# Kernel tuning notes

Measured on AMD Instinct MI355X. Metric: run time of the kernel, lower is better.

The kernel has to match this reference:

```python
import jax, jax.numpy as jnp
import numpy as np

N_NODES = 100000
N_EDGES = 1600000
IN_DIM = 128
HID = 128
OUT = 40


def setup_inputs() -> dict:
    key = jax.random.key(0)
    ks = jax.random.split(key, 8)
    x = jax.random.normal(ks[0], (N_NODES, IN_DIM), dtype=jnp.float32)
    edge_index = jax.random.randint(ks[1], (2, N_EDGES), 0, N_NODES, dtype=jnp.int64)
    def glorot(k, fan_in, fan_out):
        s = jnp.sqrt(6.0 / (fan_in + fan_out)).astype(jnp.float32)
        return jax.random.uniform(k, (fan_in, fan_out), jnp.float32, -s, s)
    return {
        "x": x,
        "edge_index": edge_index,
        "W1": glorot(ks[2], IN_DIM, HID), "b1": jnp.zeros((HID,), jnp.float32),
        "W2": glorot(ks[3], HID, HID),    "b2": jnp.zeros((HID,), jnp.float32),
        "W3": glorot(ks[4], HID, HID),    "b3": jnp.zeros((HID,), jnp.float32),
        "Wl": glorot(ks[5], HID, OUT),    "bl": jnp.zeros((OUT,), jnp.float32),
    }


def _gcn_norm(edge_index, num_nodes):
    # PyG GCNConv default: add self-loops, symmetric normalization.
    loops = jnp.arange(num_nodes, dtype=edge_index.dtype)
    src = jnp.concatenate([edge_index[0], loops])
    dst = jnp.concatenate([edge_index[1], loops])
    deg = jax.ops.segment_sum(jnp.ones_like(dst, dtype=jnp.float32), dst,
                              num_segments=num_nodes)
    dis = jnp.where(deg > 0, jax.lax.rsqrt(deg), 0.0)  # deg^{-1/2}
    norm = dis[src] * dis[dst]  # [E+N]
    return src, dst, norm


def _gcn_conv(x, W, b, src, dst, norm, num_nodes):
    h = x @ W                                   # [N, F_out]
    msg = h[src] * norm[:, None]                # gather + scale
    out = jax.ops.segment_sum(msg, dst, num_segments=num_nodes)
    return out + b


def reference(x, edge_index, W1, b1, W2, b2, W3, b3, Wl, bl):
    n = x.shape[0]
    src, dst, norm = _gcn_norm(edge_index, n)
    h = jax.nn.relu(_gcn_conv(x, W1, b1, src, dst, norm, n))
    h = jax.nn.relu(_gcn_conv(h, W2, b2, src, dst, norm, n))
    h = _gcn_conv(h, W3, b3, src, dst, norm, n)
    # dropout p=0.5 is identity in eval mode
    return h @ Wl + bl
```

## Files before the change

kernel.cpp:

```cpp
#include <hip/hip_runtime.h>

typedef __attribute__((ext_vector_type(8))) short sh8;
typedef __attribute__((ext_vector_type(4))) float f4;

__device__ __forceinline__ float bf2f(unsigned short u) {
    union { unsigned int u; float f; } c; c.u = ((unsigned int)u) << 16; return c.f;
}
__device__ __forceinline__ unsigned short f2bf(float f) {
    union { float f; unsigned int u; } c; c.f = f;
    unsigned int x = c.u;
    unsigned int r = (x + 0x7fffu + ((x >> 16) & 1u)) >> 16;
    return (unsigned short)r;
}
__device__ __forceinline__ void bfsplit(float x, short& hi, short& lo) {
    unsigned short h = f2bf(x);
    float r = x - bf2f(h);
    hi = (short)h;
    lo = (short)f2bf(r);
}

#define CG_BLOCKS 2304
#define CG_COUNT  1152
#define CSR_GRID  1568

__global__ void k_init(int* cnt8, int M,
                       const float* __restrict__ W1, const float* __restrict__ W2,
                       const float* __restrict__ W3, unsigned short* __restrict__ sp) {
    int j = blockIdx.x * 256 + threadIdx.x;
    if (j < M) cnt8[j] = 0;
    if (j < 16384) {
        int k = j >> 7, col = j & 127;
        int t = col * 128 + k;
        short h, l;
        bfsplit(W1[j], h, l); sp[t] = (unsigned short)h; sp[16384 + t] = (unsigned short)l;
        bfsplit(W2[j], h, l); sp[32768 + t] = (unsigned short)h; sp[49152 + t] = (unsigned short)l;
        bfsplit(W3[j], h, l); sp[65536 + t] = (unsigned short)h; sp[81920 + t] = (unsigned short)l;
    }
}

__device__ __forceinline__ void count_body(const int* __restrict__ dst,
                                           int* __restrict__ cnt8,
                                           int* __restrict__ rank, int E, int N) {
    int cidx = blockIdx.x >> 1;
    int base = (cidx & 7) * N;
    int E4 = E >> 2;
    for (int i = cidx * 256 + threadIdx.x; i < E4; i += CG_COUNT * 256) {
        int4 d = ((const int4*)dst)[i];
        int4 r;
        r.x = ((unsigned)d.x < (unsigned)N) ? atomicAdd(&cnt8[base + d.x], 1) : -1;
        r.y = ((unsigned)d.y < (unsigned)N) ? atomicAdd(&cnt8[base + d.y], 1) : -1;
        r.z = ((unsigned)d.z < (unsigned)N) ? atomicAdd(&cnt8[base + d.z], 1) : -1;
        r.w = ((unsigned)d.w < (unsigned)N) ? atomicAdd(&cnt8[base + d.w], 1) : -1;
        ((int4*)rank)[i] = r;
    }
    if (cidx == 0) {
        for (int e = (E4 << 2) + threadIdx.x; e < E; e += 256) {
            int d = dst[e];
            rank[e] = ((unsigned)d < (unsigned)N) ? atomicAdd(&cnt8[d], 1) : -1;
        }
    }
}

__device__ __forceinline__ void gemm1_body(const float* __restrict__ X,
                                           const unsigned short* __restrict__ Wh,
                                           const unsigned short* __restrict__ Wl,
                                           unsigned short* __restrict__ H, int nPairs) {
    int gidx = blockIdx.x >> 1;
    int wave = threadIdx.x >> 6;
    int lane = threadIdx.x & 63;
    int ln = lane & 15, quad = lane >> 4;
    int c0 = (wave & 1) * 64;
    int subTile = wave >> 1;

    for (int p = gidx; p < nPairs; p += CG_COUNT) {
        int nodeBase = p * 32 + subTile * 16;
        const float* xrow = X + (nodeBase + ln) * 128 + quad * 8;
        sh8 ah[4], al[4];
        #pragma unroll
        for (int kt = 0; kt < 4; ++kt) {
            f4 v0 = *(const f4*)(xrow + kt * 32);
            f4 v1 = *(const f4*)(xrow + kt * 32 + 4);
            #pragma unroll
            for (int j = 0; j < 4; ++j) {
                short h, l;
                bfsplit(v0[j], h, l); ah[kt][j] = h; al[kt][j] = l;
                bfsplit(v1[j], h, l); ah[kt][j + 4] = h; al[kt][j + 4] = l;
            }
        }

        f4 acc[4] = { {0.f,0.f,0.f,0.f}, {0.f,0.f,0.f,0.f}, {0.f,0.f,0.f,0.f}, {0.f,0.f,0.f,0.f} };
        #pragma unroll
        for (int kt = 0; kt < 4; ++kt) {
            int k0 = kt * 32 + quad * 8;
            #pragma unroll
            for (int nt = 0; nt < 4; ++nt) {
                int col = c0 + nt * 16 + ln;
                sh8 bh = *(const sh8*)(Wh + col * 128 + k0);
                sh8 bl = *(const sh8*)(Wl + col * 128 + k0);
                acc[nt] = __builtin_amdgcn_mfma_f32_16x16x32_bf16(ah[kt], bh, acc[nt], 0, 0, 0);
                acc[nt] = __builtin_amdgcn_mfma_f32_16x16x32_bf16(ah[kt], bl, acc[nt], 0, 0, 0);
                acc[nt] = __builtin_amdgcn_mfma_f32_16x16x32_bf16(al[kt], bh, acc[nt], 0, 0, 0);
            }
        }

        #pragma unroll
        for (int nt = 0; nt < 4; ++nt) {
            int col = c0 + nt * 16 + ln;
            #pragma unroll
            for (int r = 0; r < 4; ++r)
                H[(nodeBase + quad * 4 + r) * 128 + col] = f2bf(acc[nt][r]);
        }
    }
}

__global__ __launch_bounds__(256)
void k_count_gemm1(const int* __restrict__ dst, int* __restrict__ cnt8,
                   int* __restrict__ rank, int E, int N,
                   const float* __restrict__ X,
                   const unsigned short* __restrict__ Wh,
                   const unsigned short* __restrict__ Wl,
                   unsigned short* __restrict__ H, int nPairs) {
    if ((blockIdx.x & 1) == 0)
        count_body(dst, cnt8, rank, E, N);
    else
        gemm1_body(X, Wh, Wl, H, nPairs);
}

#define SCAN_B 256
__global__ void k_scan_a(const int* __restrict__ cnt8, int* __restrict__ rowptr,
                         int* __restrict__ off8, int* __restrict__ deg,
                         int* __restrict__ bsum, float* __restrict__ dis, int N) {
    __shared__ int sh[SCAN_B];
    int t = threadIdx.x, i = blockIdx.x * SCAN_B + t;
    int c[8];
    int v = 0;
    if (i < N) {
        #pragma unroll
        for (int g = 0; g < 8; ++g) { c[g] = cnt8[g * N + i]; v += c[g]; }
        dis[i] = rsqrtf((float)(v + 1));
        deg[i] = v;
    }
    sh[t] = v; __syncthreads();
    for (int off = 1; off < SCAN_B; off <<= 1) {
        int x = (t >= off) ? sh[t - off] : 0;
        __syncthreads();
        sh[t] += x;
        __syncthreads();
    }
    int incl = sh[t];
    if (i < N) {
        int b = incl - v;
        rowptr[i] = b;
        int o = b;
        #pragma unroll
        for (int g = 0; g < 8; ++g) { off8[g * N + i] = o; o += c[g]; }
    }
    if (t == SCAN_B - 1) bsum[blockIdx.x] = incl;
}

__global__ void k_scan_b(int* bsum, int NB) {
    __shared__ int sh[512];
    int t = threadIdx.x;
    int v = (t < NB) ? bsum[t] : 0;
    sh[t] = v; __syncthreads();
    for (int off = 1; off < 512; off <<= 1) {
        int x = (t >= off) ? sh[t - off] : 0;
        __syncthreads();
        sh[t] += x;
        __syncthreads();
    }
    if (t < NB) bsum[t] = sh[t] - v;
}

__global__ void k_scan_c(int* __restrict__ rowptr, int* __restrict__ off8,
                         const int* __restrict__ bsum, int N) {
    int i = blockIdx.x * 256 + threadIdx.x;
    if (i < N) {
        int b = bsum[blockIdx.x];
        rowptr[i] += b;
        #pragma unroll
        for (int g = 0; g < 8; ++g) off8[g * N + i] += b;
    }
}

__global__ void k_fill(const int* __restrict__ src, const int* __restrict__ dst,
                       const int* __restrict__ rank, const int* __restrict__ off8,
                       int* __restrict__ csrc, int E, int N) {
    int E4 = E >> 2;
    for (int i = blockIdx.x * 256 + threadIdx.x; i < E4; i += gridDim.x * 256) {
        int g = (i >> 8) & 7;
        const int* off = off8 + g * N;
        int4 d4 = ((const int4*)dst)[i];
        int4 s4 = ((const int4*)src)[i];
        int4 r4 = ((const int4*)rank)[i];
        #pragma unroll
        for (int q = 0; q < 4; ++q) {
            int d = (q == 0) ? d4.x : (q == 1) ? d4.y : (q == 2) ? d4.z : d4.w;
            int s = (q == 0) ? s4.x : (q == 1) ? s4.y : (q == 2) ? s4.z : s4.w;
            int r = (q == 0) ? r4.x : (q == 1) ? r4.y : (q == 2) ? r4.z : r4.w;
            if ((unsigned)d >= (unsigned)N || (unsigned)s >= (unsigned)N || r < 0) continue;
            csrc[off[d] + r] = s;
        }
    }
    if (blockIdx.x == 0) {
        for (int e = (E4 << 2) + threadIdx.x; e < E; e += 256) {
            int d = dst[e];
            int s = src[e];
            int r = rank[e];
            if ((unsigned)d >= (unsigned)N || (unsigned)s >= (unsigned)N || r < 0) continue;
            csrc[off8[d] + r] = s;
        }
    }
}

__global__ __launch_bounds__(256)
void k_gemm128_a16(const unsigned short* __restrict__ X,
                   const unsigned short* __restrict__ Wh,
                   const unsigned short* __restrict__ Wl,
                   const float* __restrict__ dis,
                   unsigned short* __restrict__ H, int nPairs) {
    int wave = threadIdx.x >> 6;
    int lane = threadIdx.x & 63;
    int ln = lane & 15, quad = lane >> 4;
    int c0 = (wave & 1) * 64;
    int subTile = wave >> 1;

    for (int p = blockIdx.x; p < nPairs; p += gridDim.x) {
        int nodeBase = p * 32 + subTile * 16;
        const unsigned short* xrow = X + (nodeBase + ln) * 128 + quad * 8;
        sh8 a[4];
        #pragma unroll
        for (int kt = 0; kt < 4; ++kt) a[kt] = *(const sh8*)(xrow + kt * 32);

        f4 acc[4] = { {0.f,0.f,0.f,0.f}, {0.f,0.f,0.f,0.f}, {0.f,0.f,0.f,0.f}, {0.f,0.f,0.f,0.f} };
        #pragma unroll
        for (int kt = 0; kt < 4; ++kt) {
            int k0 = kt * 32 + quad * 8;
            #pragma unroll
            for (int nt = 0; nt < 4; ++nt) {
                int col = c0 + nt * 16 + ln;
                sh8 bh = *(const sh8*)(Wh + col * 128 + k0);
                sh8 bl = *(const sh8*)(Wl + col * 128 + k0);
                acc[nt] = __builtin_amdgcn_mfma_f32_16x16x32_bf16(a[kt], bh, acc[nt], 0, 0, 0);
                acc[nt] = __builtin_amdgcn_mfma_f32_16x16x32_bf16(a[kt], bl, acc[nt], 0, 0, 0);
            }
        }

        float ds[4];
        #pragma unroll
        for (int r = 0; r < 4; ++r) ds[r] = dis[nodeBase + quad * 4 + r];
        #pragma unroll
        for (int nt = 0; nt < 4; ++nt) {
            int col = c0 + nt * 16 + ln;
            #pragma unroll
            for (int r = 0; r < 4; ++r)
                H[(nodeBase + quad * 4 + r) * 128 + col] = f2bf(acc[nt][r] * ds[r]);
        }
    }
}

__global__ __launch_bounds__(256)
void k_agg(const unsigned short* __restrict__ H,
           unsigned short* __restrict__ O,
           const float* __restrict__ dis,
           const int* __restrict__ rowptr,
           const int* __restrict__ deg,
           const int* __restrict__ csrc,
           const float* __restrict__ bias,
           int relu, int scaled, int N) {
    int n = (blockIdx.x * 256 + threadIdx.x) >> 5;
    if (n >= N) return;
    int lane = threadIdx.x & 31;
    int sub  = lane & 15;
    int half = lane >> 4;

    float a0 = 0.f, a1 = 0.f, a2 = 0.f, a3 = 0.f;
    float a4 = 0.f, a5 = 0.f, a6 = 0.f, a7 = 0.f;
    float dn = dis[n];

    auto addrow = [&](uint4 v) {
        a0 += bf2f((unsigned short)v.x);
        a1 += bf2f((unsigned short)(v.x >> 16));
        a2 += bf2f((unsigned short)v.y);
        a3 += bf2f((unsigned short)(v.y >> 16));
        a4 += bf2f((unsigned short)v.z);
        a5 += bf2f((unsigned short)(v.z >> 16));
        a6 += bf2f((unsigned short)v.w);
        a7 += bf2f((unsigned short)(v.w >> 16));
    };
    auto addroww = [&](uint4 v, float w) {
        a0 = fmaf(w, bf2f((unsigned short)v.x), a0);
        a1 = fmaf(w, bf2f((unsigned short)(v.x >> 16)), a1);
        a2 = fmaf(w, bf2f((unsigned short)v.y), a2);
        a3 = fmaf(w, bf2f((unsigned short)(v.y >> 16)), a3);
        a4 = fmaf(w, bf2f((unsigned short)v.z), a4);
        a5 = fmaf(w, bf2f((unsigned short)(v.z >> 16)), a5);
        a6 = fmaf(w, bf2f((unsigned short)v.w), a6);
        a7 = fmaf(w, bf2f((unsigned short)(v.w >> 16)), a7);
    };

    if (half == 0) {
        uint4 v = *(const uint4*)(H + (size_t)n * 128 + sub * 8);
        if (scaled) addrow(v); else addroww(v, dn);
    }

    int start = rowptr[n];
    int e = deg[n];
    int i = 0;
    if (scaled) {
        for (; i + 8 <= e; i += 8) {
            int s[4];
            #pragma unroll
            for (int q = 0; q < 4; ++q) s[q] = csrc[start + i + 2 * q + half];
            uint4 v[4];
            #pragma unroll
            for (int q = 0; q < 4; ++q) v[q] = *(const uint4*)(H + (size_t)s[q] * 128 + sub * 8);
            #pragma unroll
            for (int q = 0; q < 4; ++q) addrow(v[q]);
        }
        for (int j = i + half; j < e; j += 2) {
            int s = csrc[start + j];
            addrow(*(const uint4*)(H + (size_t)s * 128 + sub * 8));
        }
    } else {
        for (; i + 8 <= e; i += 8) {
            int s[4];
            #pragma unroll
            for (int q = 0; q < 4; ++q) s[q] = csrc[start + i + 2 * q + half];
            uint4 v[4];
            #pragma unroll
            for (int q = 0; q < 4; ++q) v[q] = *(const uint4*)(H + (size_t)s[q] * 128 + sub * 8);
            float w[4];
            #pragma unroll
            for (int q = 0; q < 4; ++q) w[q] = dis[s[q]];
            #pragma unroll
            for (int q = 0; q < 4; ++q) addroww(v[q], w[q]);
        }
        for (int j = i + half; j < e; j += 2) {
            int s = csrc[start + j];
            float w = dis[s];
            addroww(*(const uint4*)(H + (size_t)s * 128 + sub * 8), w);
        }
    }

    a0 += __shfl_xor(a0, 16); a1 += __shfl_xor(a1, 16);
    a2 += __shfl_xor(a2, 16); a3 += __shfl_xor(a3, 16);
    a4 += __shfl_xor(a4, 16); a5 += __shfl_xor(a5, 16);
    a6 += __shfl_xor(a6, 16); a7 += __shfl_xor(a7, 16);

    if (half == 0) {
        f4 b0 = *(const f4*)(bias + sub * 8);
        f4 b1 = *(const f4*)(bias + sub * 8 + 4);
        a0 = a0 * dn + b0[0]; a1 = a1 * dn + b0[1];
        a2 = a2 * dn + b0[2]; a3 = a3 * dn + b0[3];
        a4 = a4 * dn + b1[0]; a5 = a5 * dn + b1[1];
        a6 = a6 * dn + b1[2]; a7 = a7 * dn + b1[3];
        if (relu) {
            a0 = fmaxf(a0, 0.f); a1 = fmaxf(a1, 0.f);
            a2 = fmaxf(a2, 0.f); a3 = fmaxf(a3, 0.f);
            a4 = fmaxf(a4, 0.f); a5 = fmaxf(a5, 0.f);
            a6 = fmaxf(a6, 0.f); a7 = fmaxf(a7, 0.f);
        }
        uint4 ov;
        ov.x = (unsigned int)f2bf(a0) | ((unsigned int)f2bf(a1) << 16);
        ov.y = (unsigned int)f2bf(a2) | ((unsigned int)f2bf(a3) << 16);
        ov.z = (unsigned int)f2bf(a4) | ((unsigned int)f2bf(a5) << 16);
        ov.w = (unsigned int)f2bf(a6) | ((unsigned int)f2bf(a7) << 16);
        *(uint4*)(O + (size_t)n * 128 + sub * 8) = ov;
    }
}

__global__ __launch_bounds__(256)
void k_gemm_final(const unsigned short* __restrict__ X,
                  const float* __restrict__ W,
                  const float* __restrict__ bl,
                  float* __restrict__ OUT, int nTiles) {
    int wave = threadIdx.x >> 6;
    int lane = threadIdx.x & 63;
    int ln = lane & 15, quad = lane >> 4;
    int tile = blockIdx.x * 4 + wave;
    if (tile >= nTiles) return;

    sh8 bh[3][4], blo[3][4];
    #pragma unroll
    for (int nt = 0; nt < 3; ++nt) {
        int col = nt * 16 + ln;
        bool valid = (col < 40);
        #pragma unroll
        for (int kt = 0; kt < 4; ++kt) {
            int k0 = kt * 32 + quad * 8;
            #pragma unroll
            for (int j = 0; j < 8; ++j) {
                short h = 0, l = 0;
                if (valid) bfsplit(W[(k0 + j) * 40 + col], h, l);
                bh[nt][kt][j] = h; blo[nt][kt][j] = l;
            }
        }
    }

    int nodeBase = tile * 16;
    const unsigned short* xrow = X + (nodeBase + ln) * 128 + quad * 8;
    sh8 a[4];
    #pragma unroll
    for (int kt = 0; kt < 4; ++kt) a[kt] = *(const sh8*)(xrow + kt * 32);

    f4 acc[3] = { {0.f,0.f,0.f,0.f}, {0.f,0.f,0.f,0.f}, {0.f,0.f,0.f,0.f} };
    #pragma unroll
    for (int kt = 0; kt < 4; ++kt)
        #pragma unroll
        for (int nt = 0; nt < 3; ++nt) {
            acc[nt] = __builtin_amdgcn_mfma_f32_16x16x32_bf16(a[kt], bh[nt][kt], acc[nt], 0, 0, 0);
            acc[nt] = __builtin_amdgcn_mfma_f32_16x16x32_bf16(a[kt], blo[nt][kt], acc[nt], 0, 0, 0);
        }

    #pragma unroll
    for (int nt = 0; nt < 3; ++nt) {
        int col = nt * 16 + ln;
        if (col < 40) {
            float bv = bl[col];
            #pragma unroll
            for (int r = 0; r < 4; ++r)
                OUT[(nodeBase + quad * 4 + r) * 40 + col] = acc[nt][r] + bv;
        }
    }
}

extern "C" void kernel_launch(void* const* d_in, const int* in_sizes, int n_in,
                              void* d_out, int out_size, void* d_ws, size_t ws_size,
                              hipStream_t stream) {
    const float* x  = (const float*)d_in[0];
    const int*   ei = (const int*)d_in[1];
    const float* W1 = (const float*)d_in[2];
    const float* b1 = (const float*)d_in[3];
    const float* W2 = (const float*)d_in[4];
    const float* b2 = (const float*)d_in[5];
    const float* W3 = (const float*)d_in[6];
    const float* b3 = (const float*)d_in[7];
    const float* Wl = (const float*)d_in[8];
    const float* bl = (const float*)d_in[9];

    const int N = in_sizes[0] / 128;
    const int E = in_sizes[1] / 2;
    const int* srcIdx = ei;
    const int* dstIdx = ei + E;

    char* ws = (char*)d_ws;
    size_t off = 0;
    auto alloc = [&](size_t bytes) { void* p = ws + off; off += (bytes + 511) & ~(size_t)511; return p; };
    int*   rowptr  = (int*)  alloc((size_t)N * 4);
    int*   deg     = (int*)  alloc((size_t)N * 4);
    float* dis     = (float*)alloc((size_t)N * 4);
    int*   bsum    = (int*)  alloc(512 * 4);
    unsigned short* wsp = (unsigned short*)alloc(6 * 16384 * 2);
    int*   csrc    = (int*)  alloc((size_t)E * 4);
    unsigned short* h0 = (unsigned short*)alloc((size_t)N * 128 * 2);
    unsigned short* h1 = (unsigned short*)alloc((size_t)N * 128 * 2);
    int* rank = (int*)h1;
    int* off8 = (int*)((char*)h1 + (8u << 20));
    int* cnt8 = (int*)((char*)h1 + (16u << 20));
    unsigned short* Wh1 = wsp;
    unsigned short* Wl1 = wsp + 16384;
    unsigned short* Wh2 = wsp + 32768;
    unsigned short* Wl2 = wsp + 49152;
    unsigned short* Wh3 = wsp + 65536;
    unsigned short* Wl3 = wsp + 81920;

    const int gN = (N + 255) / 256;
    const int nPairs = N / 32;
    const int nTiles = N / 16;
    const int gAgg = (N * 32 + 255) / 256;
    const int gZ8 = (N * 8 + 255) / 256;

    k_init<<<gZ8, 256, 0, stream>>>(cnt8, N * 8, W1, W2, W3, wsp);
    k_count_gemm1<<<CG_BLOCKS, 256, 0, stream>>>(dstIdx, cnt8, rank, E, N,
                                                 x, Wh1, Wl1, h0, nPairs);
    k_scan_a<<<gN, 256, 0, stream>>>(cnt8, rowptr, off8, deg, bsum, dis, N);
    k_scan_b<<<1, 512, 0, stream>>>(bsum, gN);
    k_scan_c<<<gN, 256, 0, stream>>>(rowptr, off8, bsum, N);
    k_fill<<<CSR_GRID, 256, 0, stream>>>(srcIdx, dstIdx, rank, off8, csrc, E, N);

    k_agg<<<gAgg, 256, 0, stream>>>(h0, h1, dis, rowptr, deg, csrc, b1, 1, 0, N);
    k_gemm128_a16<<<1536, 256, 0, stream>>>(h1, Wh2, Wl2, dis, h0, nPairs);
    k_agg<<<gAgg, 256, 0, stream>>>(h0, h1, dis, rowptr, deg, csrc, b2, 1, 1, N);
    k_gemm128_a16<<<1536, 256, 0, stream>>>(h1, Wh3, Wl3, dis, h0, nPairs);
    k_agg<<<gAgg, 256, 0, stream>>>(h0, h1, dis, rowptr, deg, csrc, b3, 0, 1, N);
    k_gemm_final<<<(nTiles + 3) / 4, 256, 0, stream>>>(h1, Wl, bl, (float*)d_out, nTiles);
}
```

Measured before the change: 492.3 us.

## Fuse neighbor aggregation with the following GEMM through LDS tiles

Each block now aggregates 32 nodes' neighbor features into a swizzled LDS tile, then runs the next layer's MFMA GEMM directly from LDS. This removes the intermediate write and re-read of the aggregated activations, along with three kernel launches. The final linear head is fused with the last aggregation, and its weights are pre-split to bf16 hi/lo once in k_init. The cost is that aggregation now uses 16 lanes per node processing two nodes serially instead of 32 lanes with a shuffle reduction, which may lower memory-level parallelism in the gather phase. Half the waves also sit idle during the head GEMM.

```diff
diff --git a/kernel.cpp b/kernel.cpp
--- a/kernel.cpp
+++ b/kernel.cpp
@@ -25,7 +25,8 @@
 
 __global__ void k_init(int* cnt8, int M,
                        const float* __restrict__ W1, const float* __restrict__ W2,
-                       const float* __restrict__ W3, unsigned short* __restrict__ sp) {
+                       const float* __restrict__ W3, const float* __restrict__ WL,
+                       unsigned short* __restrict__ sp) {
     int j = blockIdx.x * 256 + threadIdx.x;
     if (j < M) cnt8[j] = 0;
     if (j < 16384) {
@@ -35,6 +36,14 @@
         bfsplit(W1[j], h, l); sp[t] = (unsigned short)h; sp[16384 + t] = (unsigned short)l;
         bfsplit(W2[j], h, l); sp[32768 + t] = (unsigned short)h; sp[49152 + t] = (unsigned short)l;
         bfsplit(W3[j], h, l); sp[65536 + t] = (unsigned short)h; sp[81920 + t] = (unsigned short)l;
+    }
+    if (j < 5120) {
+        int k = j / 40, col = j - k * 40;
+        int t = col * 128 + k;
+        short h, l;
+        bfsplit(WL[j], h, l);
+        sp[98304 + t] = (unsigned short)h;
+        sp[103424 + t] = (unsigned short)l;
     }
 }
 
@@ -213,205 +222,211 @@
     }
 }
 
+__device__ __forceinline__ void agg_to_lds(unsigned short* lds,
+        const unsigned short* __restrict__ Hsrc,
+        const float* __restrict__ dis,
+        const int* __restrict__ rowptr, const int* __restrict__ deg,
+        const int* __restrict__ csrc, const float* __restrict__ bias,
+        int relu, int scaled, int nodeBase, int N) {
+    int g = threadIdx.x >> 4;
+    int l16 = threadIdx.x & 15;
+    f4 bv0 = *(const f4*)(bias + l16 * 8);
+    f4 bv1 = *(const f4*)(bias + l16 * 8 + 4);
+
+    for (int nn = 0; nn < 2; ++nn) {
+        int nl = g * 2 + nn;
+        int n = nodeBase + nl;
+        if (n >= N) continue;
+        float dn = dis[n];
+        float a0, a1, a2, a3, a4, a5, a6, a7;
+        {
+            uint4 v = *(const uint4*)(Hsrc + (size_t)n * 128 + l16 * 8);
+            float w = scaled ? 1.f : dn;
+            a0 = w * bf2f((unsigned short)v.x);
+            a1 = w * bf2f((unsigned short)(v.x >> 16));
+            a2 = w * bf2f((unsigned short)v.y);
+            a3 = w * bf2f((unsigned short)(v.y >> 16));
+            a4 = w * bf2f((unsigned short)v.z);
+            a5 = w * bf2f((unsigned short)(v.z >> 16));
+            a6 = w * bf2f((unsigned short)v.w);
+            a7 = w * bf2f((unsigned short)(v.w >> 16));
+        }
+        auto addrow = [&](uint4 v) {
+            a0 += bf2f((unsigned short)v.x);
+            a1 += bf2f((unsigned short)(v.x >> 16));
+            a2 += bf2f((unsigned short)v.y);
+            a3 += bf2f((unsigned short)(v.y >> 16));
+            a4 += bf2f((unsigned short)v.z);
+            a5 += bf2f((unsigned short)(v.z >> 16));
+            a6 += bf2f((unsigned short)v.w);
+            a7 += bf2f((unsigned short)(v.w >> 16));
+        };
+        auto addroww = [&](uint4 v, float w) {
+            a0 = fmaf(w, bf2f((unsigned short)v.x), a0);
+            a1 = fmaf(w, bf2f((unsigned short)(v.x >> 16)), a1);
+            a2 = fmaf(w, bf2f((unsigned short)v.y), a2);
+            a3 = fmaf(w, bf2f((unsigned short)(v.y >> 16)), a3);
+            a4 = fmaf(w, bf2f((unsigned short)v.z), a4);
+            a5 = fmaf(w, bf2f((unsigned short)(v.z >> 16)), a5);
+            a6 = fmaf(w, bf2f((unsigned short)v.w), a6);
+            a7 = fmaf(w, bf2f((unsigned short)(v.w >> 16)), a7);
+        };
+
+        int start = rowptr[n];
+        int e = deg[n];
+        int i = 0;
+        if (scaled) {
+            for (; i + 8 <= e; i += 8) {
+                int s[8];
+                #pragma unroll
+                for (int q = 0; q < 8; ++q) s[q] = csrc[start + i + q];
+                uint4 v[8];
+                #pragma unroll
+                for (int q = 0; q < 8; ++q) v[q] = *(const uint4*)(Hsrc + (size_t)s[q] * 128 + l16 * 8);
+                #pragma unroll
+                for (int q = 0; q < 8; ++q) addrow(v[q]);
+            }
+            for (; i < e; ++i) {
+                int s = csrc[start + i];
+                addrow(*(const uint4*)(Hsrc + (size_t)s * 128 + l16 * 8));
+            }
+        } else {
+            for (; i + 8 <= e; i += 8) {
+                int s[8];
+                #pragma unroll
+                for (int q = 0; q < 8; ++q) s[q] = csrc[start + i + q];
+                uint4 v[8];
+                #pragma unroll
+                for (int q = 0; q < 8; ++q) v[q] = *(const uint4*)(Hsrc + (size_t)s[q] * 128 + l16 * 8);
+                float w[8];
+                #pragma unroll
+                for (int q = 0; q < 8; ++q) w[q] = dis[s[q]];
+                #pragma unroll
+                for (int q = 0; q < 8; ++q) addroww(v[q], w[q]);
+            }
+            for (; i < e; ++i) {
+                int s = csrc[start + i];
+                float w = dis[s];
+                addroww(*(const uint4*)(Hsrc + (size_t)s * 128 + l16 * 8), w);
+            }
+        }
+
+        a0 = a0 * dn + bv0[0]; a1 = a1 * dn + bv0[1];
+        a2 = a2 * dn + bv0[2]; a3 = a3 * dn + bv0[3];
+        a4 = a4 * dn + bv1[0]; a5 = a5 * dn + bv1[1];
+        a6 = a6 * dn + bv1[2]; a7 = a7 * dn + bv1[3];
+        if (relu) {
+            a0 = fmaxf(a0, 0.f); a1 = fmaxf(a1, 0.f);
+            a2 = fmaxf(a2, 0.f); a3 = fmaxf(a3, 0.f);
+            a4 = fmaxf(a4, 0.f); a5 = fmaxf(a5, 0.f);
+            a6 = fmaxf(a6, 0.f); a7 = fmaxf(a7, 0.f);
+        }
+        uint4 ov;
+        ov.x = (unsigned int)f2bf(a0) | ((unsigned int)f2bf(a1) << 16);
+        ov.y = (unsigned int)f2bf(a2) | ((unsigned int)f2bf(a3) << 16);
+        ov.z = (unsigned int)f2bf(a4) | ((unsigned int)f2bf(a5) << 16);
+        ov.w = (unsigned int)f2bf(a6) | ((unsigned int)f2bf(a7) << 16);
+        *(uint4*)((char*)lds + nl * 256 + ((l16 * 16) ^ ((nl & 7) << 4))) = ov;
+    }
+}
+
 __global__ __launch_bounds__(256)
-void k_gemm128_a16(const unsigned short* __restrict__ X,
+void k_agg_gemm128(const unsigned short* __restrict__ Hsrc,
+                   unsigned short* __restrict__ Hout,
+                   const float* __restrict__ dis,
+                   const int* __restrict__ rowptr, const int* __restrict__ deg,
+                   const int* __restrict__ csrc, const float* __restrict__ bias,
+                   int relu, int scaled,
                    const unsigned short* __restrict__ Wh,
                    const unsigned short* __restrict__ Wl,
-                   const float* __restrict__ dis,
-                   unsigned short* __restrict__ H, int nPairs) {
+                   int N) {
+    __shared__ unsigned short lds[32 * 128];
+    int nodeBase = blockIdx.x * 32;
+    agg_to_lds(lds, Hsrc, dis, rowptr, deg, csrc, bias, relu, scaled, nodeBase, N);
+    __syncthreads();
+
     int wave = threadIdx.x >> 6;
     int lane = threadIdx.x & 63;
     int ln = lane & 15, quad = lane >> 4;
     int c0 = (wave & 1) * 64;
     int subTile = wave >> 1;
-
-    for (int p = blockIdx.x; p < nPairs; p += gridDim.x) {
-        int nodeBase = p * 32 + subTile * 16;
-        const unsigned short* xrow = X + (nodeBase + ln) * 128 + quad * 8;
-        sh8 a[4];
-        #pragma unroll
-        for (int kt = 0; kt < 4; ++kt) a[kt] = *(const sh8*)(xrow + kt * 32);
-
-        f4 acc[4] = { {0.f,0.f,0.f,0.f}, {0.f,0.f,0.f,0.f}, {0.f,0.f,0.f,0.f}, {0.f,0.f,0.f,0.f} };
-        #pragma unroll
-        for (int kt = 0; kt < 4; ++kt) {
-            int k0 = kt * 32 + quad * 8;
-            #pragma unroll
-            for (int nt = 0; nt < 4; ++nt) {
-                int col = c0 + nt * 16 + ln;
-                sh8 bh = *(const sh8*)(Wh + col * 128 + k0);
-                sh8 bl = *(const sh8*)(Wl + col * 128 + k0);
-                acc[nt] = __builtin_amdgcn_mfma_f32_16x16x32_bf16(a[kt], bh, acc[nt], 0, 0, 0);
-                acc[nt] = __builtin_amdgcn_mfma_f32_16x16x32_bf16(a[kt], bl, acc[nt], 0, 0, 0);
-            }
-        }
-
-        float ds[4];
-        #pragma unroll
-        for (int r = 0; r < 4; ++r) ds[r] = dis[nodeBase + quad * 4 + r];
+    int row = subTile * 16 + ln;
+
+    sh8 a[4];
+    #pragma unroll
+    for (int kt = 0; kt < 4; ++kt)
+        a[kt] = *(const sh8*)((const char*)lds + row * 256 +
+                              ((quad * 16 + kt * 64) ^ ((row & 7) << 4)));
+
+    f4 acc[4] = { {0.f,0.f,0.f,0.f}, {0.f,0.f,0.f,0.f}, {0.f,0.f,0.f,0.f}, {0.f,0.f,0.f,0.f} };
+    #pragma unroll
+    for (int kt = 0; kt < 4; ++kt) {
+        int k0 = kt * 32 + quad * 8;
         #pragma unroll
         for (int nt = 0; nt < 4; ++nt) {
             int col = c0 + nt * 16 + ln;
-            #pragma unroll
-            for (int r = 0; r < 4; ++r)
-                H[(nodeBase + quad * 4 + r) * 128 + col] = f2bf(acc[nt][r] * ds[r]);
-        }
+            sh8 bh = *(const sh8*)(Wh + col * 128 + k0);
+            sh8 bl = *(const sh8*)(Wl + col * 128 + k0);
+            acc[nt] = __builtin_amdgcn_mfma_f32_16x16x32_bf16(a[kt], bh, acc[nt], 0, 0, 0);
+            acc[nt] = __builtin_amdgcn_mfma_f32_16x16x32_bf16(a[kt], bl, acc[nt], 0, 0, 0);
+        }
+    }
+
+    int orow0 = nodeBase + subTile * 16 + quad * 4;
+    float ds[4];
+    #pragma unroll
+    for (int r = 0; r < 4; ++r) ds[r] = (orow0 + r < N) ? dis[orow0 + r] : 0.f;
+    #pragma unroll
+    for (int nt = 0; nt < 4; ++nt) {
+        int col = c0 + nt * 16 + ln;
+        #pragma unroll
+        for (int r = 0; r < 4; ++r)
+            if (orow0 + r < N)
+                Hout[(size_t)(orow0 + r) * 128 + col] = f2bf(acc[nt][r] * ds[r]);
     }
 }
 
 __global__ __launch_bounds__(256)
-void k_agg(const unsigned short* __restrict__ H,
-           unsigned short* __restrict__ O,
-           const float* __restrict__ dis,
-           const int* __restrict__ rowptr,
-           const int* __restrict__ deg,
-           const int* __restrict__ csrc,
-           const float* __restrict__ bias,
-           int relu, int scaled, int N) {
-    int n = (blockIdx.x * 256 + threadIdx.x) >> 5;
-    if (n >= N) return;
-    int lane = threadIdx.x & 31;
-    int sub  = lane & 15;
-    int half = lane >> 4;
-
-    float a0 = 0.f, a1 = 0.f, a2 = 0.f, a3 = 0.f;
-    float a4 = 0.f, a5 = 0.f, a6 = 0.f, a7 = 0.f;
-    float dn = dis[n];
-
-    auto addrow = [&](uint4 v) {
-        a0 += bf2f((unsigned short)v.x);
-        a1 += bf2f((unsigned short)(v.x >> 16));
-        a2 += bf2f((unsigned short)v.y);
-        a3 += bf2f((unsigned short)(v.y >> 16));
-        a4 += bf2f((unsigned short)v.z);
-        a5 += bf2f((unsigned short)(v.z >> 16));
-        a6 += bf2f((unsigned short)v.w);
-        a7 += bf2f((unsigned short)(v.w >> 16));
-    };
-    auto addroww = [&](uint4 v, float w) {
-        a0 = fmaf(w, bf2f((unsigned short)v.x), a0);
-        a1 = fmaf(w, bf2f((unsigned short)(v.x >> 16)), a1);
-        a2 = fmaf(w, bf2f((unsigned short)v.y), a2);
-        a3 = fmaf(w, bf2f((unsigned short)(v.y >> 16)), a3);
-        a4 = fmaf(w, bf2f((unsigned short)v.z), a4);
-        a5 = fmaf(w, bf2f((unsigned short)(v.z >> 16)), a5);
-        a6 = fmaf(w, bf2f((unsigned short)v.w), a6);
-        a7 = fmaf(w, bf2f((unsigned short)(v.w >> 16)), a7);
-    };
-
-    if (half == 0) {
-        uint4 v = *(const uint4*)(H + (size_t)n * 128 + sub * 8);
-        if (scaled) addrow(v); else addroww(v, dn);
-    }
-
-    int start = rowptr[n];
-    int e = deg[n];
-    int i = 0;
-    if (scaled) {
-        for (; i + 8 <= e; i += 8) {
-            int s[4];
-            #pragma unroll
-            for (int q = 0; q < 4; ++q) s[q] = csrc[start + i + 2 * q + half];
-            uint4 v[4];
-            #pragma unroll
-            for (int q = 0; q < 4; ++q) v[q] = *(const uint4*)(H + (size_t)s[q] * 128 + sub * 8);
-            #pragma unroll
-            for (int q = 0; q < 4; ++q) addrow(v[q]);
-        }
-        for (int j = i + half; j < e; j += 2) {
-            int s = csrc[start + j];
-            addrow(*(const uint4*)(H + (size_t)s * 128 + sub * 8));
-        }
-    } else {
-        for (; i + 8 <= e; i += 8) {
-            int s[4];
-            #pragma unroll
-            for (int q = 0; q < 4; ++q) s[q] = csrc[start + i + 2 * q + half];
-            uint4 v[4];
-            #pragma unroll
-            for (int q = 0; q < 4; ++q) v[q] = *(const uint4*)(H + (size_t)s[q] * 128 + sub * 8);
-            float w[4];
-            #pragma unroll
-            for (int q = 0; q < 4; ++q) w[q] = dis[s[q]];
-            #pragma unroll
-            for (int q = 0; q < 4; ++q) addroww(v[q], w[q]);
-        }
-        for (int j = i + half; j < e; j += 2) {
-            int s = csrc[start + j];
-            float w = dis[s];
-            addroww(*(const uint4*)(H + (size_t)s * 128 + sub * 8), w);
-        }
-    }
-
-    a0 += __shfl_xor(a0, 16); a1 += __shfl_xor(a1, 16);
-    a2 += __shfl_xor(a2, 16); a3 += __shfl_xor(a3, 16);
-    a4 += __shfl_xor(a4, 16); a5 += __shfl_xor(a5, 16);
-    a6 += __shfl_xor(a6, 16); a7 += __shfl_xor(a7, 16);
-
-    if (half == 0) {
-        f4 b0 = *(const f4*)(bias + sub * 8);
-        f4 b1 = *(const f4*)(bias + sub * 8 + 4);
-        a0 = a0 * dn + b0[0]; a1 = a1 * dn + b0[1];
-        a2 = a2 * dn + b0[2]; a3 = a3 * dn + b0[3];
-        a4 = a4 * dn + b1[0]; a5 = a5 * dn + b1[1];
-        a6 = a6 * dn + b1[2]; a7 = a7 * dn + b1[3];
-        if (relu) {
-            a0 = fmaxf(a0, 0.f); a1 = fmaxf(a1, 0.f);
-            a2 = fmaxf(a2, 0.f); a3 = fmaxf(a3, 0.f);
-            a4 = fmaxf(a4, 0.f); a5 = fmaxf(a5, 0.f);
-            a6 = fmaxf(a6, 0.f); a7 = fmaxf(a7, 0.f);
-        }
-        uint4 ov;
-        ov.x = (unsigned int)f2bf(a0) | ((unsigned int)f2bf(a1) << 16);
-        ov.y = (unsigned int)f2bf(a2) | ((unsigned int)f2bf(a3) << 16);
-        ov.z = (unsigned int)f2bf(a4) | ((unsigned int)f2bf(a5) << 16);
-        ov.w = (unsigned int)f2bf(a6) | ((unsigned int)f2bf(a7) << 16);
-        *(uint4*)(O + (size_t)n * 128 + sub * 8) = ov;
-    }
-}
-
-__global__ __launch_bounds__(256)
-void k_gemm_final(const unsigned short* __restrict__ X,
-                  const float* __restrict__ W,
-                  const float* __restrict__ bl,
-                  float* __restrict__ OUT, int nTiles) {
+void k_agg_head(const unsigned short* __restrict__ Hsrc,
+                float* __restrict__ OUT,
+                const float* __restrict__ dis,
+                const int* __restrict__ rowptr, const int* __restrict__ deg,
+                const int* __restrict__ csrc, const float* __restrict__ bias,
+                const unsigned short* __restrict__ Wh,
+                const unsigned short* __restrict__ Wl,
+                const float* __restrict__ bl,
+                int N) {
+    __shared__ unsigned short lds[32 * 128];
+    int nodeBase = blockIdx.x * 32;
+    agg_to_lds(lds, Hsrc, dis, rowptr, deg, csrc, bias, 0, 1, nodeBase, N);
+    __syncthreads();
+
     int wave = threadIdx.x >> 6;
+    if (wave >= 2) return;
     int lane = threadIdx.x & 63;
     int ln = lane & 15, quad = lane >> 4;
-    int tile = blockIdx.x * 4 + wave;
-    if (tile >= nTiles) return;
-
-    sh8 bh[3][4], blo[3][4];
-    #pragma unroll
-    for (int nt = 0; nt < 3; ++nt) {
-        int col = nt * 16 + ln;
-        bool valid = (col < 40);
-        #pragma unroll
-        for (int kt = 0; kt < 4; ++kt) {
-            int k0 = kt * 32 + quad * 8;
-            #pragma unroll
-            for (int j = 0; j < 8; ++j) {
-                short h = 0, l = 0;
-                if (valid) bfsplit(W[(k0 + j) * 40 + col], h, l);
-                bh[nt][kt][j] = h; blo[nt][kt][j] = l;
-            }
-        }
-    }
-
-    int nodeBase = tile * 16;
-    const unsigned short* xrow = X + (nodeBase + ln) * 128 + quad * 8;
+    int row = wave * 16 + ln;
+
     sh8 a[4];
     #pragma unroll
-    for (int kt = 0; kt < 4; ++kt) a[kt] = *(const sh8*)(xrow + kt * 32);
+    for (int kt = 0; kt < 4; ++kt)
+        a[kt] = *(const sh8*)((const char*)lds + row * 256 +
+                              ((quad * 16 + kt * 64) ^ ((row & 7) << 4)));
 
     f4 acc[3] = { {0.f,0.f,0.f,0.f}, {0.f,0.f,0.f,0.f}, {0.f,0.f,0.f,0.f} };
     #pragma unroll
-    for (int kt = 0; kt < 4; ++kt)
+    for (int kt = 0; kt < 4; ++kt) {
+        int k0 = kt * 32 + quad * 8;
         #pragma unroll
         for (int nt = 0; nt < 3; ++nt) {
-            acc[nt] = __builtin_amdgcn_mfma_f32_16x16x32_bf16(a[kt], bh[nt][kt], acc[nt], 0, 0, 0);
-            acc[nt] = __builtin_amdgcn_mfma_f32_16x16x32_bf16(a[kt], blo[nt][kt], acc[nt], 0, 0, 0);
-        }
+            int col = nt * 16 + ln;
+            int colc = (col < 40) ? col : 0;
+            sh8 bh = *(const sh8*)(Wh + colc * 128 + k0);
+            sh8 bl = *(const sh8*)(Wl + colc * 128 + k0);
+            acc[nt] = __builtin_amdgcn_mfma_f32_16x16x32_bf16(a[kt], bh, acc[nt], 0, 0, 0);
+            acc[nt] = __builtin_amdgcn_mfma_f32_16x16x32_bf16(a[kt], bl, acc[nt], 0, 0, 0);
+        }
+    }
 
     #pragma unroll
     for (int nt = 0; nt < 3; ++nt) {
@@ -419,8 +434,10 @@
         if (col < 40) {
             float bv = bl[col];
             #pragma unroll
-            for (int r = 0; r < 4; ++r)
-                OUT[(nodeBase + quad * 4 + r) * 40 + col] = acc[nt][r] + bv;
+            for (int r = 0; r < 4; ++r) {
+                int orow = nodeBase + wave * 16 + quad * 4 + r;
+                if (orow < N) OUT[(size_t)orow * 40 + col] = acc[nt][r] + bv;
+            }
         }
     }
 }
@@ -451,7 +468,7 @@
     int*   deg     = (int*)  alloc((size_t)N * 4);
     float* dis     = (float*)alloc((size_t)N * 4);
     int*   bsum    = (int*)  alloc(512 * 4);
-    unsigned short* wsp = (unsigned short*)alloc(6 * 16384 * 2);
+    unsigned short* wsp = (unsigned short*)alloc(108544 * 2);
     int*   csrc    = (int*)  alloc((size_t)E * 4);
     unsigned short* h0 = (unsigned short*)alloc((size_t)N * 128 * 2);
     unsigned short* h1 = (unsigned short*)alloc((size_t)N * 128 * 2);
@@ -464,14 +481,15 @@
     unsigned short* Wl2 = wsp + 49152;
     unsigned short* Wh3 = wsp + 65536;
     unsigned short* Wl3 = wsp + 81920;
+    unsigned short* WhL = wsp + 98304;
+    unsigned short* WlL = wsp + 103424;
 
     const int gN = (N + 255) / 256;
     const int nPairs = N / 32;
-    const int nTiles = N / 16;
-    const int gAgg = (N * 32 + 255) / 256;
+    const int gL = (N + 31) / 32;
     const int gZ8 = (N * 8 + 255) / 256;
 
-    k_init<<<gZ8, 256, 0, stream>>>(cnt8, N * 8, W1, W2, W3, wsp);
+    k_init<<<gZ8, 256, 0, stream>>>(cnt8, N * 8, W1, W2, W3, Wl, wsp);
     k_count_gemm1<<<CG_BLOCKS, 256, 0, stream>>>(dstIdx, cnt8, rank, E, N,
                                                  x, Wh1, Wl1, h0, nPairs);
     k_scan_a<<<gN, 256, 0, stream>>>(cnt8, rowptr, off8, deg, bsum, dis, N);
@@ -479,10 +497,10 @@
     k_scan_c<<<gN, 256, 0, stream>>>(rowptr, off8, bsum, N);
     k_fill<<<CSR_GRID, 256, 0, stream>>>(srcIdx, dstIdx, rank, off8, csrc, E, N);
 
-    k_agg<<<gAgg, 256, 0, stream>>>(h0, h1, dis, rowptr, deg, csrc, b1, 1, 0, N);
-    k_gemm128_a16<<<1536, 256, 0, stream>>>(h1, Wh2, Wl2, dis, h0, nPairs);
-    k_agg<<<gAgg, 256, 0, stream>>>(h0, h1, dis, rowptr, deg, csrc, b2, 1, 1, N);
-    k_gemm128_a16<<<1536, 256, 0, stream>>>(h1, Wh3, Wl3, dis, h0, nPairs);
-    k_agg<<<gAgg, 256, 0, stream>>>(h0, h1, dis, rowptr, deg, csrc, b3, 0, 1, N);
-    k_gemm_final<<<(nTiles + 3) / 4, 256, 0, stream>>>(h1, Wl, bl, (float*)d_out, nTiles);
-}
+    k_agg_gemm128<<<gL, 256, 0, stream>>>(h0, h1, dis, rowptr, deg, csrc, b1, 1, 0,
+                                          Wh2, Wl2, N);
+    k_agg_gemm128<<<gL, 256, 0, stream>>>(h1, h0, dis, rowptr, deg, csrc, b2, 1, 1,
+                                          Wh3, Wl3, N);
+    k_agg_head<<<gL, 256, 0, stream>>>(h0, (float*)d_out, dis, rowptr, deg, csrc, b3,
+                                       WhL, WlL, bl, N);
+}
```

Result: slower. 567.1 us (+15.2%).
